# Performance work log

Measured on AMD Instinct MI355X. Metric: run time of the kernel, lower is better.

The kernel has to match this reference:

```python
import jax, jax.numpy as jnp
import numpy as np
from jax import lax

# Faithful JAX translation of Laplacian_Forward_Model.forward(acc=False).
# The opaque approximate multiplier (mul_wrapper) is modeled as an exact
# multiply, under which approx_sharp and accurate_sharp produce identical
# values; the original assigns x.data = approx result (values) while grads
# flow through the accurate path, so with exact multiply the single accurate
# path (with straight-through floor) reproduces the full forward math.

LAPLACIAN = np.array([-1.0, -1.0, -1.0, -1.0, 8.0, -1.0, -1.0, -1.0, -1.0]) / 8.0


def setup_inputs() -> dict:
    key = jax.random.key(0)
    k_in, = jax.random.split(key, 1)
    B = 16384
    n_mult = 1  # len(mul_approx_func_arr)
    inp = jax.random.uniform(k_in, (B, 1, 32, 32), dtype=jnp.float32) * 255.0
    weight = jnp.asarray(np.tile(LAPLACIAN, (n_mult, 1)), dtype=jnp.float32)          # (n_mult, 9)
    weight_factor = jnp.asarray(np.tile(np.array([8.0]), (n_mult, 1)), dtype=jnp.float32)  # (n_mult, 1)
    return {"input": inp, "weight": weight, "weight_factor": weight_factor}


def _sharp(x, ker):
    # depthwise 3x3 conv, padding 1 (C=1 so plain conv)
    B = x.shape[0]
    conv = lax.conv_general_dilated(x, ker, window_strides=(1, 1),
                                    padding=((1, 1), (1, 1)),
                                    dimension_numbers=("NCHW", "OIHW", "NCHW"))
    flat = conv.reshape(B, -1)
    cmax = lax.stop_gradient(flat.max(axis=1)).reshape(B, 1, 1, 1)
    cmin = lax.stop_gradient(flat.min(axis=1)).reshape(B, 1, 1, 1)
    mod = (conv - cmin) / jnp.maximum(cmax - cmin, 1e-6) * 255.0
    sharpened = x + mod
    sflat = sharpened.reshape(B, -1)
    smax = lax.stop_gradient(sflat.max(axis=1)).reshape(B, 1, 1, 1)
    smin = lax.stop_gradient(sflat.min(axis=1)).reshape(B, 1, 1, 1)
    res = jnp.clip((sharpened - smin) / jnp.clip(smax - smin, 1e-6, 255.0) * 255.0, 0.0, 255.0)
    # result.data = floor(result.data): straight-through floor
    return res + lax.stop_gradient(jnp.floor(res) - res)


def reference(input, weight, weight_factor):
    n_mult = weight.shape[0]
    outs = []
    for ii in range(n_mult):  # small fixed loop over approx-multiplier variants
        wc = jnp.clip(weight[ii], -0.999, 0.999)            # clamp + hardtanh(-1,1)
        wf = jnp.clip(weight_factor[ii], 1.001, 254.999)    # clamp + hardtanh(1,255)
        ker = (wc * wf).reshape(1, 1, 3, 3).astype(input.dtype)
        outs.append(_sharp(input, ker))
    return jnp.stack(outs, 0)  # (n_mult, B, 1, 32, 32)
```

## Files before the change

kernel.cpp:

```cpp
#include <hip/hip_runtime.h>
#include <math.h>


#define S 36
#define SLICE 1228

typedef float floatx4 __attribute__((ext_vector_type(4)));

template <int CTRL>
__device__ __forceinline__ float dppmov(float x) {
    return __int_as_float(__builtin_amdgcn_update_dpp(
        __float_as_int(x), __float_as_int(x), CTRL, 0xf, 0xf, false));
}

template <int CTRL>
__device__ __forceinline__ float dppsh0(float x) {
    return __int_as_float(__builtin_amdgcn_update_dpp(
        0, __float_as_int(x), CTRL, 0xf, 0xf, true));
}

__device__ __forceinline__ void wave64_minmax(float& mn, float& mx) {
    mn = fminf(mn, dppmov<0x111>(mn)); mx = fmaxf(mx, dppmov<0x111>(mx));
    mn = fminf(mn, dppmov<0x112>(mn)); mx = fmaxf(mx, dppmov<0x112>(mx));
    mn = fminf(mn, dppmov<0x114>(mn)); mx = fmaxf(mx, dppmov<0x114>(mx));
    mn = fminf(mn, dppmov<0x118>(mn)); mx = fmaxf(mx, dppmov<0x118>(mx));
    mn = fminf(mn, dppmov<0x142>(mn)); mx = fmaxf(mx, dppmov<0x142>(mx));
    mn = fminf(mn, dppmov<0x143>(mn)); mx = fmaxf(mx, dppmov<0x143>(mx));
}

__device__ __forceinline__ float rd63(float v) {
    return __int_as_float(__builtin_amdgcn_readlane(__float_as_int(v), 63));
}

__device__ __forceinline__ void local_minmax16(const float v[4][4],
                                               float& mn, float& mx) {
    mn = v[0][0]; mx = v[0][0];
#pragma unroll
    for (int i = 0; i < 4; ++i)
#pragma unroll
        for (int j = 0; j < 4; ++j) {
            mn = fminf(mn, v[i][j]);
            mx = fmaxf(mx, v[i][j]);
        }
}

__device__ __forceinline__ void finish_image(
    const float4* __restrict__ x4, float conv[4][4],
    float* __restrict__ dst, int lane)
{
    float mn, mx;
    local_minmax16(conv, mn, mx);
    wave64_minmax(mn, mx);
    const float cmin = rd63(mn), cmax = rd63(mx);
    const float inv1 = 255.0f / fmaxf(cmax - cmin, 1e-6f);
    float sh[4][4];
#pragma unroll
    for (int i = 0; i < 4; ++i) {
        sh[i][0] = x4[i].x + (conv[i][0] - cmin) * inv1;
        sh[i][1] = x4[i].y + (conv[i][1] - cmin) * inv1;
        sh[i][2] = x4[i].z + (conv[i][2] - cmin) * inv1;
        sh[i][3] = x4[i].w + (conv[i][3] - cmin) * inv1;
    }
    local_minmax16(sh, mn, mx);
    wave64_minmax(mn, mx);
    const float smin = rd63(mn), smax = rd63(mx);
    const float inv2 = 255.0f / fminf(fmaxf(smax - smin, 1e-6f), 255.0f);
    const float c2 = -smin * inv2;
#pragma unroll
    for (int i = 0; i < 4; ++i) {
        floatx4 o;
        o.x = floorf(fminf(fmaxf(sh[i][0] * inv2 + c2, 0.0f), 255.0f));
        o.y = floorf(fminf(fmaxf(sh[i][1] * inv2 + c2, 0.0f), 255.0f));
        o.z = floorf(fminf(fmaxf(sh[i][2] * inv2 + c2, 0.0f), 255.0f));
        o.w = floorf(fminf(fmaxf(sh[i][3] * inv2 + c2, 0.0f), 255.0f));
        __builtin_nontemporal_store(o, (floatx4*)(dst + i * 256 + lane * 4));
    }
}

__device__ __forceinline__ void fast_image(
    float* __restrict__ sm, const float4* __restrict__ x4,
    float k0, float dk, float* __restrict__ dst, int lane)
{
    const int rbase = lane >> 3;
    const int col0  = (lane & 7) << 2;
    const bool ledge = (lane & 7) == 0;
    const bool redge = (lane & 7) == 7;

    float4 rs[4];
    __builtin_amdgcn_wave_barrier();
#pragma unroll
    for (int i = 0; i < 4; ++i) {
        const float4 m = x4[i];
        float lv = dppsh0<0x138>(m.w);
        float rv = dppsh0<0x130>(m.x);
        lv = ledge ? 0.0f : lv;
        rv = redge ? 0.0f : rv;
        const float t1 = m.x + m.y, t2 = m.z + m.w;
        rs[i].x = lv + t1; rs[i].y = t1 + m.z;
        rs[i].z = m.y + t2; rs[i].w = t2 + rv;
        *(float4*)&sm[(i * 8 + rbase + 1) * S + (col0 + 4)] = rs[i];
    }
    __builtin_amdgcn_wave_barrier();

    float conv[4][4];
#pragma unroll
    for (int i = 0; i < 4; ++i) {
        const int row = i * 8 + rbase;
        const float4 top = *(const float4*)&sm[ row      * S + col0 + 4];
        const float4 bot = *(const float4*)&sm[(row + 2) * S + col0 + 4];
        conv[i][0] = (top.x + rs[i].x + bot.x) * k0 + dk * x4[i].x;
        conv[i][1] = (top.y + rs[i].y + bot.y) * k0 + dk * x4[i].y;
        conv[i][2] = (top.z + rs[i].z + bot.z) * k0 + dk * x4[i].z;
        conv[i][3] = (top.w + rs[i].w + bot.w) * k0 + dk * x4[i].w;
    }
    __builtin_amdgcn_wave_barrier();

    finish_image(x4, conv, dst, lane);
}

__device__ __forceinline__ void gen_image(
    float* __restrict__ sm, const float4* __restrict__ x4, const float* k,
    float* __restrict__ dst, int lane)
{
    const int rbase = lane >> 3;
    const int col0  = (lane & 7) << 2;

    __builtin_amdgcn_wave_barrier();
#pragma unroll
    for (int i = 0; i < 4; ++i)
        *(float4*)&sm[(i * 8 + rbase + 1) * S + (col0 + 4)] = x4[i];
    __builtin_amdgcn_wave_barrier();

    float conv[4][4];
#pragma unroll
    for (int i = 0; i < 4; ++i) {
        const int row = i * 8 + rbase;
        const float* pt = &sm[ row      * S + col0];
        const float* pm = &sm[(row + 1) * S + col0];
        const float* pb = &sm[(row + 2) * S + col0];
        const float  tl = pt[3], tr = pt[8];
        const float4 tm = *(const float4*)(pt + 4);
        const float  ml = pm[3], mr = pm[8];
        const float  bl = pb[3], br = pb[8];
        const float4 bm = *(const float4*)(pb + 4);
        const float4 m  = x4[i];
        conv[i][0] = k[0]*tl   + k[1]*tm.x + k[2]*tm.y
                   + k[3]*ml   + k[4]*m.x  + k[5]*m.y
                   + k[6]*bl   + k[7]*bm.x + k[8]*bm.y;
        conv[i][1] = k[0]*tm.x + k[1]*tm.y + k[2]*tm.z
                   + k[3]*m.x  + k[4]*m.y  + k[5]*m.z
                   + k[6]*bm.x + k[7]*bm.y + k[8]*bm.z;
        conv[i][2] = k[0]*tm.y + k[1]*tm.z + k[2]*tm.w
                   + k[3]*m.y  + k[4]*m.z  + k[5]*m.w
                   + k[6]*bm.y + k[7]*bm.z + k[8]*bm.w;
        conv[i][3] = k[0]*tm.z + k[1]*tm.w + k[2]*tr
                   + k[3]*m.z  + k[4]*m.w  + k[5]*mr
                   + k[6]*bm.z + k[7]*bm.w + k[8]*br;
    }
    __builtin_amdgcn_wave_barrier();

    finish_image(x4, conv, dst, lane);
}

__global__ __launch_bounds__(256) void laplacian_fwd_kernel(
    const float* __restrict__ in,
    const float* __restrict__ weight,
    const float* __restrict__ wfac,
    float* __restrict__ out)
{
    __shared__ float lds[4 * SLICE];

    const int t    = threadIdx.x;
    const int w    = t >> 6;
    const int lane = t & 63;
    float* sm = &lds[w * SLICE];

    const int wave_id = blockIdx.x * 4 + w;
    const size_t base = (size_t)wave_id * 4096;

    float4 x[4];
#pragma unroll
    for (int i = 0; i < 4; ++i)
        x[i] = *(const float4*)(in + base + i * 256 + lane * 4);

    if (lane < 36) { sm[lane] = 0.0f; sm[33 * S + lane] = 0.0f; }
    if (lane < 32) { sm[(lane + 1) * S] = 0.0f; sm[(lane + 1) * S + 3] = 0.0f; }
    if (lane == 0) sm[34 * S] = 0.0f;

    const float wf = fminf(fmaxf(wfac[0], 1.001f), 254.999f);
    float k[9];
#pragma unroll
    for (int i = 0; i < 9; ++i)
        k[i] = fminf(fmaxf(weight[i], -0.999f), 0.999f) * wf;

    const bool fast = (k[0] == k[1]) && (k[0] == k[2]) && (k[0] == k[3]) &&
                      (k[0] == k[5]) && (k[0] == k[6]) && (k[0] == k[7]) &&
                      (k[0] == k[8]);

    if (fast) {
        const float k0 = k[0];
        const float dk = k[4] - k[0];
#pragma unroll
        for (int im = 0; im < 4; ++im) {
            float4 xn[4];
            if (im < 3) {
#pragma unroll
                for (int i = 0; i < 4; ++i)
                    xn[i] = *(const float4*)(in + base + (im + 1) * 1024 +
                                             i * 256 + lane * 4);
            }
            fast_image(sm, x, k0, dk, out + base + im * 1024, lane);
            if (im < 3) {
#pragma unroll
                for (int i = 0; i < 4; ++i) x[i] = xn[i];
            }
        }
    } else {
#pragma unroll
        for (int im = 0; im < 4; ++im) {
            float4 xn[4];
            if (im < 3) {
#pragma unroll
                for (int i = 0; i < 4; ++i)
                    xn[i] = *(const float4*)(in + base + (im + 1) * 1024 +
                                             i * 256 + lane * 4);
            }
            gen_image(sm, x, k, out + base + im * 1024, lane);
            if (im < 3) {
#pragma unroll
                for (int i = 0; i < 4; ++i) x[i] = xn[i];
            }
        }
    }
}

extern "C" void kernel_launch(void* const* d_in, const int* in_sizes, int n_in,
                              void* d_out, int out_size, void* d_ws, size_t ws_size,
                              hipStream_t stream) {
    const float* in   = (const float*)d_in[0];
    const float* w    = (const float*)d_in[1];
    const float* wfac = (const float*)d_in[2];
    float* out = (float*)d_out;
    const int B = in_sizes[0] / 1024;
    const int nblocks = B / 16;
    laplacian_fwd_kernel<<<nblocks, 256, 0, stream>>>(in, w, wfac, out);
}
```

Baseline: 113.6 us.

## Process one image per wave instead of four with software prefetch

```diff
diff --git a/kernel.cpp b/kernel.cpp
--- a/kernel.cpp
+++ b/kernel.cpp
@@ -53,15 +53,14 @@
     wave64_minmax(mn, mx);
     const float cmin = rd63(mn), cmax = rd63(mx);
     const float inv1 = 255.0f / fmaxf(cmax - cmin, 1e-6f);
-    float sh[4][4];
 #pragma unroll
     for (int i = 0; i < 4; ++i) {
-        sh[i][0] = x4[i].x + (conv[i][0] - cmin) * inv1;
-        sh[i][1] = x4[i].y + (conv[i][1] - cmin) * inv1;
-        sh[i][2] = x4[i].z + (conv[i][2] - cmin) * inv1;
-        sh[i][3] = x4[i].w + (conv[i][3] - cmin) * inv1;
+        conv[i][0] = x4[i].x + (conv[i][0] - cmin) * inv1;
+        conv[i][1] = x4[i].y + (conv[i][1] - cmin) * inv1;
+        conv[i][2] = x4[i].z + (conv[i][2] - cmin) * inv1;
+        conv[i][3] = x4[i].w + (conv[i][3] - cmin) * inv1;
     }
-    local_minmax16(sh, mn, mx);
+    local_minmax16(conv, mn, mx);
     wave64_minmax(mn, mx);
     const float smin = rd63(mn), smax = rd63(mx);
     const float inv2 = 255.0f / fminf(fmaxf(smax - smin, 1e-6f), 255.0f);
@@ -69,100 +68,15 @@
 #pragma unroll
     for (int i = 0; i < 4; ++i) {
         floatx4 o;
-        o.x = floorf(fminf(fmaxf(sh[i][0] * inv2 + c2, 0.0f), 255.0f));
-        o.y = floorf(fminf(fmaxf(sh[i][1] * inv2 + c2, 0.0f), 255.0f));
-        o.z = floorf(fminf(fmaxf(sh[i][2] * inv2 + c2, 0.0f), 255.0f));
-        o.w = floorf(fminf(fmaxf(sh[i][3] * inv2 + c2, 0.0f), 255.0f));
+        o.x = floorf(fminf(fmaxf(conv[i][0] * inv2 + c2, 0.0f), 255.0f));
+        o.y = floorf(fminf(fmaxf(conv[i][1] * inv2 + c2, 0.0f), 255.0f));
+        o.z = floorf(fminf(fmaxf(conv[i][2] * inv2 + c2, 0.0f), 255.0f));
+        o.w = floorf(fminf(fmaxf(conv[i][3] * inv2 + c2, 0.0f), 255.0f));
         __builtin_nontemporal_store(o, (floatx4*)(dst + i * 256 + lane * 4));
     }
 }
 
-__device__ __forceinline__ void fast_image(
-    float* __restrict__ sm, const float4* __restrict__ x4,
-    float k0, float dk, float* __restrict__ dst, int lane)
-{
-    const int rbase = lane >> 3;
-    const int col0  = (lane & 7) << 2;
-    const bool ledge = (lane & 7) == 0;
-    const bool redge = (lane & 7) == 7;
-
-    float4 rs[4];
-    __builtin_amdgcn_wave_barrier();
-#pragma unroll
-    for (int i = 0; i < 4; ++i) {
-        const float4 m = x4[i];
-        float lv = dppsh0<0x138>(m.w);
-        float rv = dppsh0<0x130>(m.x);
-        lv = ledge ? 0.0f : lv;
-        rv = redge ? 0.0f : rv;
-        const float t1 = m.x + m.y, t2 = m.z + m.w;
-        rs[i].x = lv + t1; rs[i].y = t1 + m.z;
-        rs[i].z = m.y + t2; rs[i].w = t2 + rv;
-        *(float4*)&sm[(i * 8 + rbase + 1) * S + (col0 + 4)] = rs[i];
-    }
-    __builtin_amdgcn_wave_barrier();
-
-    float conv[4][4];
-#pragma unroll
-    for (int i = 0; i < 4; ++i) {
-        const int row = i * 8 + rbase;
-        const float4 top = *(const float4*)&sm[ row      * S + col0 + 4];
-        const float4 bot = *(const float4*)&sm[(row + 2) * S + col0 + 4];
-        conv[i][0] = (top.x + rs[i].x + bot.x) * k0 + dk * x4[i].x;
-        conv[i][1] = (top.y + rs[i].y + bot.y) * k0 + dk * x4[i].y;
-        conv[i][2] = (top.z + rs[i].z + bot.z) * k0 + dk * x4[i].z;
-        conv[i][3] = (top.w + rs[i].w + bot.w) * k0 + dk * x4[i].w;
-    }
-    __builtin_amdgcn_wave_barrier();
-
-    finish_image(x4, conv, dst, lane);
-}
-
-__device__ __forceinline__ void gen_image(
-    float* __restrict__ sm, const float4* __restrict__ x4, const float* k,
-    float* __restrict__ dst, int lane)
-{
-    const int rbase = lane >> 3;
-    const int col0  = (lane & 7) << 2;
-
-    __builtin_amdgcn_wave_barrier();
-#pragma unroll
-    for (int i = 0; i < 4; ++i)
-        *(float4*)&sm[(i * 8 + rbase + 1) * S + (col0 + 4)] = x4[i];
-    __builtin_amdgcn_wave_barrier();
-
-    float conv[4][4];
-#pragma unroll
-    for (int i = 0; i < 4; ++i) {
-        const int row = i * 8 + rbase;
-        const float* pt = &sm[ row      * S + col0];
-        const float* pm = &sm[(row + 1) * S + col0];
-        const float* pb = &sm[(row + 2) * S + col0];
-        const float  tl = pt[3], tr = pt[8];
-        const float4 tm = *(const float4*)(pt + 4);
-        const float  ml = pm[3], mr = pm[8];
-        const float  bl = pb[3], br = pb[8];
-        const float4 bm = *(const float4*)(pb + 4);
-        const float4 m  = x4[i];
-        conv[i][0] = k[0]*tl   + k[1]*tm.x + k[2]*tm.y
-                   + k[3]*ml   + k[4]*m.x  + k[5]*m.y
-                   + k[6]*bl   + k[7]*bm.x + k[8]*bm.y;
-        conv[i][1] = k[0]*tm.x + k[1]*tm.y + k[2]*tm.z
-                   + k[3]*m.x  + k[4]*m.y  + k[5]*m.z
-                   + k[6]*bm.x + k[7]*bm.y + k[8]*bm.z;
-        conv[i][2] = k[0]*tm.y + k[1]*tm.z + k[2]*tm.w
-                   + k[3]*m.y  + k[4]*m.z  + k[5]*m.w
-                   + k[6]*bm.y + k[7]*bm.z + k[8]*bm.w;
-        conv[i][3] = k[0]*tm.z + k[1]*tm.w + k[2]*tr
-                   + k[3]*m.z  + k[4]*m.w  + k[5]*mr
-                   + k[6]*bm.z + k[7]*bm.w + k[8]*br;
-    }
-    __builtin_amdgcn_wave_barrier();
-
-    finish_image(x4, conv, dst, lane);
-}
-
-__global__ __launch_bounds__(256) void laplacian_fwd_kernel(
+__global__ __launch_bounds__(256, 6) void laplacian_fwd_kernel(
     const float* __restrict__ in,
     const float* __restrict__ weight,
     const float* __restrict__ wfac,
@@ -175,13 +89,20 @@
     const int lane = t & 63;
     float* sm = &lds[w * SLICE];
 
-    const int wave_id = blockIdx.x * 4 + w;
-    const size_t base = (size_t)wave_id * 4096;
-
-    float4 x[4];
+    const int img = blockIdx.x * 4 + w;
+    const size_t base = (size_t)img * 1024;
+    const float* src = in + base;
+    float* dst = out + base;
+
+    const int rbase = lane >> 3;
+    const int col0  = (lane & 7) << 2;
+    const bool ledge = (lane & 7) == 0;
+    const bool redge = (lane & 7) == 7;
+
+    float4 x4[4];
 #pragma unroll
     for (int i = 0; i < 4; ++i)
-        x[i] = *(const float4*)(in + base + i * 256 + lane * 4);
+        x4[i] = *(const float4*)(src + i * 256 + lane * 4);
 
     if (lane < 36) { sm[lane] = 0.0f; sm[33 * S + lane] = 0.0f; }
     if (lane < 32) { sm[(lane + 1) * S] = 0.0f; sm[(lane + 1) * S + 3] = 0.0f; }
@@ -197,41 +118,75 @@
                       (k[0] == k[5]) && (k[0] == k[6]) && (k[0] == k[7]) &&
                       (k[0] == k[8]);
 
+    float conv[4][4];
+
     if (fast) {
         const float k0 = k[0];
         const float dk = k[4] - k[0];
-#pragma unroll
-        for (int im = 0; im < 4; ++im) {
-            float4 xn[4];
-            if (im < 3) {
-#pragma unroll
-                for (int i = 0; i < 4; ++i)
-                    xn[i] = *(const float4*)(in + base + (im + 1) * 1024 +
-                                             i * 256 + lane * 4);
-            }
-            fast_image(sm, x, k0, dk, out + base + im * 1024, lane);
-            if (im < 3) {
-#pragma unroll
-                for (int i = 0; i < 4; ++i) x[i] = xn[i];
-            }
-        }
+
+        float4 rs[4];
+        __builtin_amdgcn_wave_barrier();
+#pragma unroll
+        for (int i = 0; i < 4; ++i) {
+            const float4 m = x4[i];
+            float lv = dppsh0<0x138>(m.w);
+            float rv = dppsh0<0x130>(m.x);
+            lv = ledge ? 0.0f : lv;
+            rv = redge ? 0.0f : rv;
+            const float t1 = m.x + m.y, t2 = m.z + m.w;
+            rs[i].x = lv + t1; rs[i].y = t1 + m.z;
+            rs[i].z = m.y + t2; rs[i].w = t2 + rv;
+            *(float4*)&sm[(i * 8 + rbase + 1) * S + (col0 + 4)] = rs[i];
+        }
+        __builtin_amdgcn_wave_barrier();
+
+#pragma unroll
+        for (int i = 0; i < 4; ++i) {
+            const int row = i * 8 + rbase;
+            const float4 top = *(const float4*)&sm[ row      * S + col0 + 4];
+            const float4 bot = *(const float4*)&sm[(row + 2) * S + col0 + 4];
+            conv[i][0] = (top.x + rs[i].x + bot.x) * k0 + dk * x4[i].x;
+            conv[i][1] = (top.y + rs[i].y + bot.y) * k0 + dk * x4[i].y;
+            conv[i][2] = (top.z + rs[i].z + bot.z) * k0 + dk * x4[i].z;
+            conv[i][3] = (top.w + rs[i].w + bot.w) * k0 + dk * x4[i].w;
+        }
+        __builtin_amdgcn_wave_barrier();
     } else {
-#pragma unroll
-        for (int im = 0; im < 4; ++im) {
-            float4 xn[4];
-            if (im < 3) {
-#pragma unroll
-                for (int i = 0; i < 4; ++i)
-                    xn[i] = *(const float4*)(in + base + (im + 1) * 1024 +
-                                             i * 256 + lane * 4);
-            }
-            gen_image(sm, x, k, out + base + im * 1024, lane);
-            if (im < 3) {
-#pragma unroll
-                for (int i = 0; i < 4; ++i) x[i] = xn[i];
-            }
-        }
+        __builtin_amdgcn_wave_barrier();
+#pragma unroll
+        for (int i = 0; i < 4; ++i)
+            *(float4*)&sm[(i * 8 + rbase + 1) * S + (col0 + 4)] = x4[i];
+        __builtin_amdgcn_wave_barrier();
+
+#pragma unroll
+        for (int i = 0; i < 4; ++i) {
+            const int row = i * 8 + rbase;
+            const float* pt = &sm[ row      * S + col0];
+            const float* pm = &sm[(row + 1) * S + col0];
+            const float* pb = &sm[(row + 2) * S + col0];
+            const float  tl = pt[3], tr = pt[8];
+            const float4 tm = *(const float4*)(pt + 4);
+            const float  ml = pm[3], mr = pm[8];
+            const float  bl = pb[3], br = pb[8];
+            const float4 bm = *(const float4*)(pb + 4);
+            const float4 m  = x4[i];
+            conv[i][0] = k[0]*tl   + k[1]*tm.x + k[2]*tm.y
+                       + k[3]*ml   + k[4]*m.x  + k[5]*m.y
+                       + k[6]*bl   + k[7]*bm.x + k[8]*bm.y;
+            conv[i][1] = k[0]*tm.x + k[1]*tm.y + k[2]*tm.z
+                       + k[3]*m.x  + k[4]*m.y  + k[5]*m.z
+                       + k[6]*bm.x + k[7]*bm.y + k[8]*bm.z;
+            conv[i][2] = k[0]*tm.y + k[1]*tm.z + k[2]*tm.w
+                       + k[3]*m.y  + k[4]*m.z  + k[5]*m.w
+                       + k[6]*bm.y + k[7]*bm.z + k[8]*bm.w;
+            conv[i][3] = k[0]*tm.z + k[1]*tm.w + k[2]*tr
+                       + k[3]*m.z  + k[4]*m.w  + k[5]*mr
+                       + k[6]*bm.z + k[7]*bm.w + k[8]*br;
+        }
+        __builtin_amdgcn_wave_barrier();
     }
+
+    finish_image(x4, conv, dst, lane);
 }
 
 extern "C" void kernel_launch(void* const* d_in, const int* in_sizes, int n_in,
@@ -242,6 +197,6 @@
     const float* wfac = (const float*)d_in[2];
     float* out = (float*)d_out;
     const int B = in_sizes[0] / 1024;
-    const int nblocks = B / 16;
+    const int nblocks = B / 4;
     laplacian_fwd_kernel<<<nblocks, 256, 0, stream>>>(in, w, wfac, out);
 }
```

New measurement: 110.0 us. 1.03x faster.
